# Optimization experiments

Hardware: AMD Instinct MI355X
Metric: run time of the kernel (lower is better)

The kernel has to match this reference:

```python
import jax, jax.numpy as jnp
import numpy as np

B, N, D, E = 64, 512, 256, 128   # batch, n_nodes, node_model_dim, edge_model_dim
N_ITERS = 20                      # max_iter_sinkhorn with fixed_n_iters=True


def setup_inputs() -> dict:
    key = jax.random.key(0)
    ks = jax.random.split(key, 9)
    return {
        "node_embeddings_inputs": jax.random.normal(ks[0], (B, N, D), jnp.float32),
        "node_masks_inputs": jax.random.randint(ks[1], (B, N), 0, 2).astype(bool),
        "node_embeddings_outputs": jax.random.normal(ks[2], (B, N, D), jnp.float32),
        # learned parameters
        "node_padding_features": jax.random.normal(ks[3], (1, 1, D), jnp.float32),
        "positional_encoding_outputs": jax.random.normal(ks[4], (1, N, D), jnp.float32),
        # stand-in for the (externally defined) EvoformerSetMatching pair stack:
        # a bilinear pair-affinity head, followed by the module's own linear_aff
        "W_a": jax.random.normal(ks[5], (D, E), jnp.float32) / np.sqrt(D),
        "W_b": jax.random.normal(ks[6], (D, E), jnp.float32) / np.sqrt(D),
        "w_aff": jax.random.normal(ks[7], (E,), jnp.float32) / np.sqrt(E),  # linear_aff weight
        "b_aff": jnp.zeros((), jnp.float32),                                # linear_aff bias
    }


def _sinkhorn(K, n_iters):
    # Fixed-iteration Sinkhorn projection toward a doubly-stochastic matrix:
    # alternately normalize columns (dim=2 sums) and rows (dim=1 sums).
    def step(P, _):
        P = P / jnp.sum(P, axis=2, keepdims=True)  # row-normalize over inputs axis
        P = P / jnp.sum(P, axis=1, keepdims=True)  # col-normalize over outputs axis
        return P, None
    P, _ = jax.lax.scan(step, K, None, length=n_iters)
    return P


def reference(node_embeddings_inputs, node_masks_inputs, node_embeddings_outputs,
              node_padding_features, positional_encoding_outputs,
              W_a, W_b, w_aff, b_aff):
    # replace padded input nodes with the learned padding feature
    mask = node_masks_inputs[..., None]                              # [B, N, 1]
    x_in = jnp.where(mask, node_padding_features, node_embeddings_inputs)
    # add positional encoding to output nodes (add_positionnal_outputs=True)
    x_out = node_embeddings_outputs + positional_encoding_outputs

    # pairwise affinity: aff[b, i(out), j(in)]  (linear_aff fused into the contraction
    # so the [B,N,N,E] pair tensor is never materialized)
    a = (x_out @ W_a) * w_aff                                        # [B, N, E]
    b = x_in @ W_b                                                   # [B, N, E]
    aff = jnp.einsum('bie,bje->bij', a, b) + b_aff                   # [B, N, N]

    # approximate doubly-stochastic init: average of the two marginal softmaxes
    K = 0.5 * jax.nn.softmax(aff, axis=1) + 0.5 * jax.nn.softmax(aff, axis=2)
    return _sinkhorn(K, N_ITERS)
```

## Files before the change

kernel.cpp:

```cpp
#include <hip/hip_runtime.h>
#include <cstddef>

static constexpr int CB = 64;
static constexpr int CN = 512;
static constexpr int CD = 256;
static constexpr int CE = 128;
static constexpr int CIT = 20;

typedef _Float16 half_t;
typedef __attribute__((ext_vector_type(8))) _Float16 v8h;
typedef __attribute__((ext_vector_type(4))) _Float16 v4h;
typedef __attribute__((ext_vector_type(4))) float v4f;

__device__ __forceinline__ void llc_store4(v4f* p, v4f v) {
  asm volatile("global_store_dwordx4 %0, %1, off sc0 sc1"
               :: "v"(p), "v"(v) : "memory");
}
__device__ __forceinline__ void llc_storef(float* p, float v) {
  asm volatile("global_store_dword %0, %1, off sc0 sc1"
               :: "v"(p), "v"(v) : "memory");
}
__device__ __forceinline__ void llc_load3x4(const v4f* p0, const v4f* p1,
                                            const v4f* p2,
                                            v4f& a, v4f& b, v4f& c) {
  asm volatile("global_load_dwordx4 %0, %3, off sc0 sc1\n\t"
               "global_load_dwordx4 %1, %4, off sc0 sc1\n\t"
               "global_load_dwordx4 %2, %5, off sc0 sc1\n\t"
               "s_waitcnt vmcnt(0)"
               : "=&v"(a), "=&v"(b), "=&v"(c)
               : "v"(p0), "v"(p1), "v"(p2)
               : "memory");
}
__device__ __forceinline__ void llc_load3f(const float* p0, const float* p1,
                                           const float* p2,
                                           float& a, float& b, float& c) {
  asm volatile("global_load_dword %0, %3, off sc0 sc1\n\t"
               "global_load_dword %1, %4, off sc0 sc1\n\t"
               "global_load_dword %2, %5, off sc0 sc1\n\t"
               "s_waitcnt vmcnt(0)"
               : "=&v"(a), "=&v"(b), "=&v"(c)
               : "v"(p0), "v"(p1), "v"(p2)
               : "memory");
}
__device__ __forceinline__ bool allpos(v4f v) {
  return v[0] > 0.0f && v[1] > 0.0f && v[2] > 0.0f && v[3] > 0.0f;
}

__global__ __launch_bounds__(512) void k0_init(
    const void* __restrict__ mask, int* __restrict__ flag,
    const float* __restrict__ W_a, const float* __restrict__ W_b,
    const float* __restrict__ w_aff,
    half_t* __restrict__ WaF, half_t* __restrict__ WbF,
    float4* __restrict__ clearp, int nclear4) {
  const int tid = threadIdx.x;
  const int blk = blockIdx.x;
  if (blk == 1) return;
  if (blk >= 18) {
    const int idx = (blk - 18) * 512 + tid;
    if (idx < nclear4)
      clearp[idx] = make_float4(-1.0f, -1.0f, -1.0f, -1.0f);
    return;
  }
  if (blk >= 2) {
    const bool is_a = (blk < 10);
    const float* W = is_a ? W_a : W_b;
    half_t* WF = is_a ? WaF : WbF;
    const int e = (blk - (is_a ? 2 : 10)) * 512 + tid;
    const int fB = e >> 6, lane = e & 63;
    const int nn = fB >> 3, kf = fB & 7;
    const int col = nn * 16 + (lane & 15);
    const int q = lane >> 4;
    const float scale = is_a ? w_aff[col] : 1.0f;
    v8h hv;
#pragma unroll
    for (int j = 0; j < 8; ++j) {
      const int k = kf * 32 + q * 8 + j;
      hv[j] = (half_t)(W[(size_t)k * CE + col] * scale);
    }
    *(v8h*)&WF[(size_t)e * 8] = hv;
    return;
  }
  __shared__ int cnt[5];
  if (tid < 5) cnt[tid] = 0;
  __syncthreads();
  const unsigned char* p = (const unsigned char*)mask;
  int l0 = 0, l1 = 0, l2 = 0, l3 = 0, l4 = 0;
  const int base = tid * 64;
  for (int k = 0; k < 64; ++k) {
    const int off = base + k;
    if (p[off]) {
      const int m4 = off & 3;
      if (m4 == 1) l1++;
      else if (m4 == 2) l2++;
      else if (m4 == 3) l3++;
      else if ((off & 7) == 4) l4++;
      else l0++;
    }
  }
  if (l0) atomicAdd(&cnt[0], 1);
  if (l1) atomicAdd(&cnt[1], 1);
  if (l2) atomicAdd(&cnt[2], 1);
  if (l3) atomicAdd(&cnt[3], 1);
  if (l4) atomicAdd(&cnt[4], 1);
  __syncthreads();
  if (tid == 0) {
    int f;
    if (cnt[1]) f = 1;
    else if (cnt[2] || cnt[3]) f = 2;
    else if (cnt[4]) f = 0;
    else if (cnt[0]) f = 3;
    else f = 1;
    *flag = f;
  }
}

__global__ __launch_bounds__(512, 2) void mega(
    const float* __restrict__ out_emb, const float* __restrict__ pos,
    const float* __restrict__ in_emb, const float* __restrict__ pad,
    const void* __restrict__ maskp, const int* __restrict__ flagp,
    const half_t* __restrict__ WaF, const half_t* __restrict__ WbF,
    half_t* __restrict__ Bm_h,
    const float* __restrict__ baff, float* __restrict__ P,
    float* __restrict__ partInit, float* __restrict__ partIter,
    float* __restrict__ markers) {
  __shared__ __align__(16) char smem2[34816];
  __shared__ __align__(16) float2 w12[512];
  __shared__ __align__(16) float QsL[512];
  __shared__ __align__(16) v4f csinv4[128];
  __shared__ __align__(16) half_t wAll[1056];
  half_t* bounce = (half_t*)smem2;
  float (*comb2)[512][2] = (float (*)[512][2])smem2;

  const int tid = threadIdx.x;
  const int wv = tid >> 6, ln = tid & 63;
  const int q = ln >> 4, l = ln & 15;
  const int b = blockIdx.x & 63;
  const int slab = blockIdx.x >> 6;
  const int i0 = slab * 128;
  const float bbs = *baff - 2.7725887f;

  int rs3[3];
  {
    int k = 0;
#pragma unroll
    for (int sl = 0; sl < 4; ++sl)
      if (sl != slab) rs3[k++] = sl;
  }

  v8h af[4];
  {
    const int row = wv * 16 + l;
    const size_t xr = ((size_t)b * CN + i0 + row) * CD;
    const size_t pr = (size_t)(i0 + row) * CD;
    v8h xf[8];
#pragma unroll
    for (int kf = 0; kf < 8; ++kf) {
      const int c = kf * 32 + q * 8;
      float4 a0 = *(const float4*)&out_emb[xr + c];
      float4 a1 = *(const float4*)&out_emb[xr + c + 4];
      const float4 p0 = *(const float4*)&pos[pr + c];
      const float4 p1 = *(const float4*)&pos[pr + c + 4];
      a0.x += p0.x; a0.y += p0.y; a0.z += p0.z; a0.w += p0.w;
      a1.x += p1.x; a1.y += p1.y; a1.z += p1.z; a1.w += p1.w;
      v8h h;
      h[0] = (half_t)a0.x; h[1] = (half_t)a0.y;
      h[2] = (half_t)a0.z; h[3] = (half_t)a0.w;
      h[4] = (half_t)a1.x; h[5] = (half_t)a1.y;
      h[6] = (half_t)a1.z; h[7] = (half_t)a1.w;
      xf[kf] = h;
    }
    v4f acc[8] = {};
#pragma unroll
    for (int nn = 0; nn < 8; ++nn)
#pragma unroll
      for (int kf = 0; kf < 8; ++kf) {
        const v8h bw = *(const v8h*)&WaF[(size_t)((nn * 8 + kf) * 64 + ln) * 8];
        acc[nn] = __builtin_amdgcn_mfma_f32_16x16x32_f16(xf[kf], bw, acc[nn], 0, 0, 0);
      }
#pragma unroll
    for (int nn = 0; nn < 8; ++nn)
#pragma unroll
      for (int g = 0; g < 4; ++g)
        bounce[(size_t)(wv * 16 + q * 4 + g) * 136 + nn * 16 + l] = (half_t)acc[nn][g];
  }
  __syncthreads();
#pragma unroll
  for (int ki = 0; ki < 4; ++ki)
    af[ki] = *(const v8h*)&bounce[(size_t)(wv * 16 + l) * 136 + ki * 32 + q * 8];
  __syncthreads();

  {
    const int flag = *flagp;
    const int row = wv * 16 + l;
    const int grow = b * CN + i0 + row;
    bool m;
    if (flag == 1)      m = ((const unsigned char*)maskp)[grow] != 0;
    else if (flag == 2) m = ((const float*)maskp)[grow] != 0.0f;
    else if (flag == 3) m = ((const long long*)maskp)[grow] != 0;
    else                m = ((const int*)maskp)[grow] != 0;
    const size_t xr = (size_t)grow * CD;
    v8h xf[8];
#pragma unroll
    for (int kf = 0; kf < 8; ++kf) {
      const int c = kf * 32 + q * 8;
      float4 a0, a1;
      if (m) {
        a0 = *(const float4*)&pad[c];
        a1 = *(const float4*)&pad[c + 4];
      } else {
        a0 = *(const float4*)&in_emb[xr + c];
        a1 = *(const float4*)&in_emb[xr + c + 4];
      }
      v8h h;
      h[0] = (half_t)a0.x; h[1] = (half_t)a0.y;
      h[2] = (half_t)a0.z; h[3] = (half_t)a0.w;
      h[4] = (half_t)a1.x; h[5] = (half_t)a1.y;
      h[6] = (half_t)a1.z; h[7] = (half_t)a1.w;
      xf[kf] = h;
    }
    v4f acc[8] = {};
#pragma unroll
    for (int nn = 0; nn < 8; ++nn)
#pragma unroll
      for (int kf = 0; kf < 8; ++kf) {
        const v8h bw = *(const v8h*)&WbF[(size_t)((nn * 8 + kf) * 64 + ln) * 8];
        acc[nn] = __builtin_amdgcn_mfma_f32_16x16x32_f16(xf[kf], bw, acc[nn], 0, 0, 0);
      }
#pragma unroll
    for (int nn = 0; nn < 8; ++nn)
#pragma unroll
      for (int g = 0; g < 4; ++g)
        bounce[(size_t)(wv * 16 + q * 4 + g) * 136 + nn * 16 + l] = (half_t)acc[nn][g];
  }
  __syncthreads();
  {
    const int row = tid >> 2, qt = tid & 3;
    half_t* dst = &Bm_h[((size_t)b * CN + i0 + row) * CE + qt * 32];
    const half_t* src = &bounce[(size_t)row * 136 + qt * 32];
#pragma unroll
    for (int j = 0; j < 4; ++j)
      llc_store4((v4f*)&dst[j * 8], *(const v4f*)&src[j * 8]);
  }
  __syncthreads();
  if (tid == 0) llc_storef(&markers[(size_t)b * 4 + slab], 1.0f);

  {
    const float* mk = &markers[(size_t)b * 4];
    float m0, m1, m2;
    while (true) {
      llc_load3f(&mk[rs3[0]], &mk[rs3[1]], &mk[rs3[2]], m0, m1, m2);
      if (m0 > 0.0f && m1 > 0.0f && m2 > 0.0f) break;
      __builtin_amdgcn_s_sleep(1);
    }
  }

  v4h eh[32];
  v4h ehT[32];
  {
    const half_t* Bbase = &Bm_h[(size_t)b * CN * CE];
#pragma unroll
    for (int ct = 0; ct < 32; ++ct) {
      v8h bf[4];
      const half_t* Brow = &Bbase[(size_t)(ct * 16 + l) * CE];
#pragma unroll
      for (int ki = 0; ki < 4; ++ki)
        bf[ki] = *(const v8h*)&Brow[ki * 32 + q * 8];
      v4f acc = {}, accT = {};
#pragma unroll
      for (int ki = 0; ki < 4; ++ki) {
        acc  = __builtin_amdgcn_mfma_f32_16x16x32_f16(af[ki], bf[ki], acc,  0, 0, 0);
        accT = __builtin_amdgcn_mfma_f32_16x16x32_f16(bf[ki], af[ki], accT, 0, 0, 0);
      }
#pragma unroll
      for (int g = 0; g < 4; ++g) {
        eh[ct][g]  = (half_t)__expf(acc[g]  + bbs);
        ehT[ct][g] = (half_t)__expf(accT[g] + bbs);
      }
    }
  }

  v4h ones;
  ones[0] = (half_t)1.0f; ones[1] = (half_t)1.0f;
  ones[2] = (half_t)1.0f; ones[3] = (half_t)1.0f;
  v4f rowacc0 = {}, rowacc1 = {};
#pragma unroll
  for (int ct = 0; ct < 32; ct += 2) {
    const v4f c0 = __builtin_amdgcn_mfma_f32_16x16x16f16(ones, eh[ct], (v4f){}, 0, 0, 0);
    const v4f c1 = __builtin_amdgcn_mfma_f32_16x16x16f16(ones, eh[ct + 1], (v4f){}, 0, 0, 0);
    if (ln < 16) {
      comb2[wv][ct * 16 + ln][0] = c0[0];
      comb2[wv][(ct + 1) * 16 + ln][0] = c1[0];
    }
    rowacc0 = __builtin_amdgcn_mfma_f32_16x16x16f16(ones, ehT[ct],     rowacc0, 0, 0, 0);
    rowacc1 = __builtin_amdgcn_mfma_f32_16x16x16f16(ones, ehT[ct + 1], rowacc1, 0, 0, 0);
  }
  const float rowtot = rowacc0[0] + rowacc1[0];
  float rv[4];
#pragma unroll
  for (int g = 0; g < 4; ++g)
    rv[g] = 1.0f / __shfl(rowtot, q * 4 + g);
  __syncthreads();

  {
    float S = 0.0f;
#pragma unroll
    for (int w = 0; w < 8; ++w) S += comb2[w][tid][0];
    QsL[tid] = S;
  }
  __syncthreads();
  if (tid < 128) {
    const v4f s4 = *(const v4f*)&QsL[tid * 4];
    v4f* pi4 = (v4f*)partInit + (size_t)b * 4 * 128;
    llc_store4(&pi4[slab * 128 + tid], s4);
    const v4f* q0 = &pi4[rs3[0] * 128 + tid];
    const v4f* q1 = &pi4[rs3[1] * 128 + tid];
    const v4f* q2 = &pi4[rs3[2] * 128 + tid];
    v4f r0, r1, r2;
    while (true) {
      llc_load3x4(q0, q1, q2, r0, r1, r2);
      if (allpos(r0) && allpos(r1) && allpos(r2)) break;
      __builtin_amdgcn_s_sleep(1);
    }
    const v4f T = s4 + r0 + r1 + r2;
    v4f ci;
    v4h w1v, w2v;
#pragma unroll
    for (int j = 0; j < 4; ++j) {
      ci[j] = 1.0f / T[j];
      w1v[j] = (half_t)(0.5f * ci[j]);
      w2v[j] = (half_t)1.0f;
    }
    csinv4[tid] = ci;
    *(v4h*)&wAll[tid * 4] = w1v;
    *(v4h*)&wAll[544 + tid * 4] = w2v;
  }
  __syncthreads();
  const float ci0 = ((const float*)csinv4)[tid];

  const half_t* wbase = (l == 1) ? (wAll + 544) : wAll;
  float u_[4], uri[4];
  for (int t = 0; t < CIT; ++t) {
    __syncthreads();
    v4f Pe = {}, Po = {};
#pragma unroll
    for (int ct = 0; ct < 32; ct += 2) {
      const v4h wf0 = *(const v4h*)&wbase[ct * 16 + q * 4];
      const v4h wf1 = *(const v4h*)&wbase[(ct + 1) * 16 + q * 4];
      Pe = __builtin_amdgcn_mfma_f32_16x16x16f16(wf0, ehT[ct],     Pe, 0, 0, 0);
      Po = __builtin_amdgcn_mfma_f32_16x16x16f16(wf1, ehT[ct + 1], Po, 0, 0, 0);
    }
    const float Prow1 = Pe[0] + Po[0];
    const float Prow2 = Pe[1] + Po[1];
    v4h u_h, uri_h;
#pragma unroll
    for (int g = 0; g < 4; ++g) {
      const float p1 = __shfl(Prow1, q * 4 + g);
      const float p2 = __shfl(Prow2, q * 4 + g);
      u_[g] = 1.0f / (p1 + 0.5f * rv[g] * p2);
      uri[g] = u_[g] * rv[g];
      u_h[g] = (half_t)u_[g];
      uri_h[g] = (half_t)uri[g];
    }
    const v4h a2 = (l == 1) ? uri_h : u_h;
#pragma unroll
    for (int ct = 0; ct < 32; ++ct) {
      const v4f s = __builtin_amdgcn_mfma_f32_16x16x16f16(a2, eh[ct], (v4f){}, 0, 0, 0);
      if (ln < 16)
        *(float2*)&comb2[wv][ct * 16 + ln][0] = make_float2(s[0], s[1]);
    }
    __syncthreads();
    {
      float S1 = 0.0f, S2 = 0.0f;
#pragma unroll
      for (int w = 0; w < 8; ++w) {
        const float2 c2v = *(const float2*)&comb2[w][tid][0];
        S1 += c2v.x;
        S2 += c2v.y;
      }
      QsL[tid] = 0.5f * fmaf(ci0, S1, S2);
    }
    __syncthreads();
    if (tid < 128) {
      const v4f Q4 = *(const v4f*)&QsL[tid * 4];
      v4f* pr4 = (v4f*)partIter + (((size_t)t * 64 + b) * 4) * 128;
      llc_store4(&pr4[slab * 128 + tid], Q4);
      const v4f* q0 = &pr4[rs3[0] * 128 + tid];
      const v4f* q1 = &pr4[rs3[1] * 128 + tid];
      const v4f* q2 = &pr4[rs3[2] * 128 + tid];
      v4f r0, r1, r2;
      while (true) {
        llc_load3x4(q0, q1, q2, r0, r1, r2);
        if (allpos(r0) && allpos(r1) && allpos(r2)) break;
        __builtin_amdgcn_s_sleep(1);
      }
      const v4f tot = Q4 + r0 + r1 + r2;
      const v4f ci = csinv4[tid];
      v4h w1v, w2v;
#pragma unroll
      for (int j = 0; j < 4; ++j) {
        const float vv = 1.0f / tot[j];
        w1v[j] = (half_t)(0.5f * vv * ci[j]);
        w2v[j] = (half_t)vv;
        if (t == CIT - 1)
          w12[tid * 4 + j] = make_float2(0.5f * vv * ci[j], vv);
      }
      *(v4h*)&wAll[tid * 4] = w1v;
      *(v4h*)&wAll[544 + tid * 4] = w2v;
    }
  }

  __syncthreads();
  float* Pb = &P[((size_t)b * CN + i0 + wv * 16 + q * 4) * CN];
#pragma unroll
  for (int ct = 0; ct < 32; ++ct) {
    const float2 w = w12[ct * 16 + l];
    const float c1 = w.x;
    const float c2 = 0.5f * w.y;
#pragma unroll
    for (int g = 0; g < 4; ++g) {
      const float e = (float)eh[ct][g];
      Pb[(size_t)g * CN + ct * 16 + l] = e * fmaf(u_[g], c1, uri[g] * c2);
    }
  }
}

extern "C" void kernel_launch(void* const* d_in, const int* in_sizes, int n_in,
                              void* d_out, int out_size, void* d_ws, size_t ws_size,
                              hipStream_t stream) {
  const float* in_emb  = (const float*)d_in[0];
  const void*  mask    = d_in[1];
  const float* out_emb = (const float*)d_in[2];
  const float* pad     = (const float*)d_in[3];
  const float* pos     = (const float*)d_in[4];
  const float* W_a     = (const float*)d_in[5];
  const float* W_b     = (const float*)d_in[6];
  const float* w_aff   = (const float*)d_in[7];
  const float* b_aff   = (const float*)d_in[8];
  float* P = (float*)d_out;

  char* ws = (char*)d_ws;
  const size_t MB = 1024 * 1024;
  const size_t KB = 1024;
  half_t* Bm_h = (half_t*)ws;
  int*    flag = (int*)(ws + 8 * MB);
  half_t* WaF  = (half_t*)(ws + 8 * MB + 16 * KB);
  half_t* WbF  = (half_t*)(ws + 8 * MB + 80 * KB);
  float* partInit = (float*)(ws + 9 * MB);
  float* partIter = (float*)(ws + 9 * MB + 512 * KB);
  float* markers  = (float*)(ws + 9 * MB + 512 * KB + 10 * MB);

  const int nclear4 = (512 * 1024 + 10 * 1024 * 1024 + 1024) / 16;
  const int nclrblk = (nclear4 + 511) / 512;

  k0_init<<<dim3(18 + nclrblk), dim3(512), 0, stream>>>(
      mask, flag, W_a, W_b, w_aff, WaF, WbF, (float4*)partInit, nclear4);
  mega<<<dim3(256), dim3(512), 0, stream>>>(
      out_emb, pos, in_emb, pad, mask, flag, WaF, WbF, Bm_h,
      b_aff, P, partInit, partIter, markers);
}
```

Before: 306.2 us.

## Replace sentinel-cleared partial buffers with monotonic per-slab epoch markers

Cross-block synchronisation in the fused kernel used to poll the partial-sum buffers until they held positive values. That required clearing about 10.5 MB of workspace to -1 in the init kernel on every launch. Each slab now publishes a monotonically increasing epoch marker after its partial sums are written, and peers wait on the markers before reading the partials. This removes the large clear and its extra init blocks. It adds a flag store, an extra barrier and a spin per phase, and it relies on correct memory ordering between the data store and the marker store.

```diff
diff --git a/kernel.cpp b/kernel.cpp
--- a/kernel.cpp
+++ b/kernel.cpp
@@ -31,19 +31,21 @@
                : "v"(p0), "v"(p1), "v"(p2)
                : "memory");
 }
-__device__ __forceinline__ void llc_load3f(const float* p0, const float* p1,
-                                           const float* p2,
-                                           float& a, float& b, float& c) {
-  asm volatile("global_load_dword %0, %3, off sc0 sc1\n\t"
-               "global_load_dword %1, %4, off sc0 sc1\n\t"
-               "global_load_dword %2, %5, off sc0 sc1\n\t"
+__device__ __forceinline__ float llc_loadf(const float* p) {
+  float v;
+  asm volatile("global_load_dword %0, %1, off sc0 sc1\n\t"
                "s_waitcnt vmcnt(0)"
-               : "=&v"(a), "=&v"(b), "=&v"(c)
-               : "v"(p0), "v"(p1), "v"(p2)
-               : "memory");
-}
-__device__ __forceinline__ bool allpos(v4f v) {
-  return v[0] > 0.0f && v[1] > 0.0f && v[2] > 0.0f && v[3] > 0.0f;
+               : "=v"(v) : "v"(p) : "memory");
+  return v;
+}
+__device__ __forceinline__ void wait_marker(const float* mk, int rsl, int ln,
+                                            float target) {
+  while (true) {
+    float f = 1e30f;
+    if (ln < 3) f = llc_loadf(&mk[rsl]);
+    if (__all(f > target)) break;
+    __builtin_amdgcn_s_sleep(1);
+  }
 }
 
 __global__ __launch_bounds__(512) void k0_init(
@@ -51,14 +53,12 @@
     const float* __restrict__ W_a, const float* __restrict__ W_b,
     const float* __restrict__ w_aff,
     half_t* __restrict__ WaF, half_t* __restrict__ WbF,
-    float4* __restrict__ clearp, int nclear4) {
+    float4* __restrict__ markers4) {
   const int tid = threadIdx.x;
   const int blk = blockIdx.x;
-  if (blk == 1) return;
-  if (blk >= 18) {
-    const int idx = (blk - 18) * 512 + tid;
-    if (idx < nclear4)
-      clearp[idx] = make_float4(-1.0f, -1.0f, -1.0f, -1.0f);
+  if (blk == 1) {
+    if (tid < CB * 4 / 4)
+      markers4[tid] = make_float4(-1.0f, -1.0f, -1.0f, -1.0f);
     return;
   }
   if (blk >= 2) {
@@ -146,6 +146,8 @@
     for (int sl = 0; sl < 4; ++sl)
       if (sl != slab) rs3[k++] = sl;
   }
+  const int rsl = (ln < 3) ? (ln + (ln >= slab ? 1 : 0)) : 0;
+  float* mk = &markers[(size_t)b * 4];
 
   v8h af[4];
   {
@@ -240,19 +242,12 @@
 #pragma unroll
     for (int j = 0; j < 4; ++j)
       llc_store4((v4f*)&dst[j * 8], *(const v4f*)&src[j * 8]);
-  }
-  __syncthreads();
-  if (tid == 0) llc_storef(&markers[(size_t)b * 4 + slab], 1.0f);
-
-  {
-    const float* mk = &markers[(size_t)b * 4];
-    float m0, m1, m2;
-    while (true) {
-      llc_load3f(&mk[rs3[0]], &mk[rs3[1]], &mk[rs3[2]], m0, m1, m2);
-      if (m0 > 0.0f && m1 > 0.0f && m2 > 0.0f) break;
-      __builtin_amdgcn_s_sleep(1);
-    }
-  }
+    asm volatile("s_waitcnt vmcnt(0)" ::: "memory");
+  }
+  __syncthreads();
+  if (tid == 0) llc_storef(&mk[slab], 1.0f);
+
+  wait_marker(mk, rsl, ln, 0.5f);
 
   v4h eh[32];
   v4h ehT[32];
@@ -308,19 +303,21 @@
     QsL[tid] = S;
   }
   __syncthreads();
+  v4f s4 = {};
   if (tid < 128) {
-    const v4f s4 = *(const v4f*)&QsL[tid * 4];
+    s4 = *(const v4f*)&QsL[tid * 4];
     v4f* pi4 = (v4f*)partInit + (size_t)b * 4 * 128;
     llc_store4(&pi4[slab * 128 + tid], s4);
-    const v4f* q0 = &pi4[rs3[0] * 128 + tid];
-    const v4f* q1 = &pi4[rs3[1] * 128 + tid];
-    const v4f* q2 = &pi4[rs3[2] * 128 + tid];
+    asm volatile("s_waitcnt vmcnt(0)" ::: "memory");
+  }
+  __syncthreads();
+  if (tid < 128) {
+    if (tid == 0) llc_storef(&mk[slab], 2.0f);
+    wait_marker(mk, rsl, ln, 1.5f);
+    v4f* pi4 = (v4f*)partInit + (size_t)b * 4 * 128;
     v4f r0, r1, r2;
-    while (true) {
-      llc_load3x4(q0, q1, q2, r0, r1, r2);
-      if (allpos(r0) && allpos(r1) && allpos(r2)) break;
-      __builtin_amdgcn_s_sleep(1);
-    }
+    llc_load3x4(&pi4[rs3[0] * 128 + tid], &pi4[rs3[1] * 128 + tid],
+                &pi4[rs3[2] * 128 + tid], r0, r1, r2);
     const v4f T = s4 + r0 + r1 + r2;
     v4f ci;
     v4h w1v, w2v;
@@ -380,19 +377,21 @@
       QsL[tid] = 0.5f * fmaf(ci0, S1, S2);
     }
     __syncthreads();
+    v4f Q4 = {};
     if (tid < 128) {
-      const v4f Q4 = *(const v4f*)&QsL[tid * 4];
+      Q4 = *(const v4f*)&QsL[tid * 4];
       v4f* pr4 = (v4f*)partIter + (((size_t)t * 64 + b) * 4) * 128;
       llc_store4(&pr4[slab * 128 + tid], Q4);
-      const v4f* q0 = &pr4[rs3[0] * 128 + tid];
-      const v4f* q1 = &pr4[rs3[1] * 128 + tid];
-      const v4f* q2 = &pr4[rs3[2] * 128 + tid];
+      asm volatile("s_waitcnt vmcnt(0)" ::: "memory");
+    }
+    __syncthreads();
+    if (tid < 128) {
+      if (tid == 0) llc_storef(&mk[slab], 3.0f + (float)t);
+      wait_marker(mk, rsl, ln, 2.5f + (float)t);
+      v4f* pr4 = (v4f*)partIter + (((size_t)t * 64 + b) * 4) * 128;
       v4f r0, r1, r2;
-      while (true) {
-        llc_load3x4(q0, q1, q2, r0, r1, r2);
-        if (allpos(r0) && allpos(r1) && allpos(r2)) break;
-        __builtin_amdgcn_s_sleep(1);
-      }
+      llc_load3x4(&pr4[rs3[0] * 128 + tid], &pr4[rs3[1] * 128 + tid],
+                  &pr4[rs3[2] * 128 + tid], r0, r1, r2);
       const v4f tot = Q4 + r0 + r1 + r2;
       const v4f ci = csinv4[tid];
       v4h w1v, w2v;
@@ -449,11 +448,8 @@
   float* partIter = (float*)(ws + 9 * MB + 512 * KB);
   float* markers  = (float*)(ws + 9 * MB + 512 * KB + 10 * MB);
 
-  const int nclear4 = (512 * 1024 + 10 * 1024 * 1024 + 1024) / 16;
-  const int nclrblk = (nclear4 + 511) / 512;
-
-  k0_init<<<dim3(18 + nclrblk), dim3(512), 0, stream>>>(
-      mask, flag, W_a, W_b, w_aff, WaF, WbF, (float4*)partInit, nclear4);
+  k0_init<<<dim3(18), dim3(512), 0, stream>>>(
+      mask, flag, W_a, W_b, w_aff, WaF, WbF, (float4*)markers);
   mega<<<dim3(256), dim3(512), 0, stream>>>(
       out_emb, pos, in_emb, pad, mask, flag, WaF, WbF, Bm_h,
       b_aff, P, partInit, partIter, markers);
```

New measurement: 305.9 us. Within noise of the previous version (-0.1%).
